# Optimization experiments

Measured on AMD Instinct MI355X. Metric: run time of the kernel, lower is better.

Reference implementation:

```python
import jax, jax.numpy as jnp
import numpy as np

B = 16       # number of point clouds
N_PER = 2048 # points per cloud
K = 16       # knn neighbors (loop=True -> self included as nearest)
NUM_CLASSES = 10


def _linear_params(key, fan_in, fan_out):
    # torch.nn.Linear default init: U(-1/sqrt(fan_in), 1/sqrt(fan_in))
    kw, kb = jax.random.split(key)
    s = 1.0 / np.sqrt(fan_in)
    W = jax.random.uniform(kw, (fan_in, fan_out), jnp.float32, -s, s)
    b = jax.random.uniform(kb, (fan_out,), jnp.float32, -s, s)
    return W, b


def setup_inputs() -> dict:
    key = jax.random.key(0)
    ks = jax.random.split(key, 7)
    pos = jax.random.normal(ks[0], (B * N_PER, 3), jnp.float32)
    batch = jnp.repeat(jnp.arange(B, dtype=jnp.int64), N_PER)  # sorted graph ids
    W1a, b1a = _linear_params(ks[1], 3 + 3, 32)   # conv1 mlp layer 1 (h=pos -> 3+3)
    W1b, b1b = _linear_params(ks[2], 32, 32)      # conv1 mlp layer 2
    W2a, b2a = _linear_params(ks[3], 32 + 3, 32)  # conv2 mlp layer 1
    W2b, b2b = _linear_params(ks[4], 32, 32)      # conv2 mlp layer 2
    Wc, bc = _linear_params(ks[5], 32, NUM_CLASSES)
    return dict(pos=pos, batch=batch,
                W1a=W1a, b1a=b1a, W1b=W1b, b1b=b1b,
                W2a=W2a, b2a=b2a, W2b=W2b, b2b=b2b,
                Wc=Wc, bc=bc)


def _knn_idx(p):
    # p: [n,3] -> [n,K] indices of K nearest points (self included, dist 0)
    d2 = jnp.sum((p[:, None, :] - p[None, :, :]) ** 2, axis=-1)  # [n,n]
    _, idx = jax.lax.top_k(-d2, K)
    return idx


def _pointnet_layer(h, p, idx, Wa, ba, Wb, bb):
    # single graph: h [n,C], p [n,3], idx [n,K]
    h_j = h[idx]                           # gather neighbor features [n,K,C]
    spatial = p[idx] - p[:, None, :]       # pos_j - pos_i [n,K,3]
    x = jnp.concatenate([h_j, spatial], axis=-1)
    x = jax.nn.relu(x @ Wa + ba) @ Wb + bb # per-edge MLP
    return jnp.max(x, axis=1)              # max aggregation over neighbors


def reference(pos, batch, W1a, b1a, W1b, b1b, W2a, b2a, W2b, b2b, Wc, bc):
    # batch is sorted with equal-sized graphs -> reshape to [B, n, 3]
    p = pos.reshape(B, N_PER, 3)
    idx = jax.vmap(_knn_idx)(p)  # [B, n, K] dynamic knn graph
    layer = jax.vmap(_pointnet_layer, in_axes=(0, 0, 0, None, None, None, None))
    h = jax.nn.relu(layer(p, p, idx, W1a, b1a, W1b, b1b))   # [B, n, 32]
    h = jax.nn.relu(layer(h, p, idx, W2a, b2a, W2b, b2b))   # [B, n, 32]
    g = jnp.max(h, axis=1)                                   # global_max_pool [B, 32]
    return g @ Wc + bc                                       # [B, num_classes]
```

## Files before the change

kernel.cpp:

```cpp
#include <hip/hip_runtime.h>
#include <hip/hip_bf16.h>
#include <cstdint>

#define NCLOUDS 16
#define N_PER   2048
#define KNN_K   16
#define CAP     48

typedef unsigned long long u64;
typedef __attribute__((ext_vector_type(8))) short bf16x8;
typedef __attribute__((ext_vector_type(4))) float f32x4;
#define INFF __builtin_inff()

template <int J>
__device__ __forceinline__ int ixor(int x) {
    if constexpr (J == 1)
        return __builtin_amdgcn_update_dpp(0, x, 0xB1, 0xF, 0xF, true);
    else if constexpr (J == 2)
        return __builtin_amdgcn_update_dpp(0, x, 0x4E, 0xF, 0xF, true);
    else if constexpr (J <= 16)
        return __builtin_amdgcn_ds_swizzle(x, (J << 10) | 0x1F);
    else
        return __shfl_xor(x, 32);
}
template <int J> __device__ __forceinline__ float fxor(float x) {
    return __int_as_float(ixor<J>(__float_as_int(x)));
}
template <int J> __device__ __forceinline__ u64 uxor(u64 x) {
    const int lo = ixor<J>((int)(x & 0xffffffffULL));
    const int hi = ixor<J>((int)(x >> 32));
    return ((u64)(unsigned)hi << 32) | (unsigned)lo;
}

__device__ __forceinline__ unsigned short f2bf(float f) {
    const unsigned u = __float_as_uint(f);
    const unsigned r = 0x7fffu + ((u >> 16) & 1u);
    return (unsigned short)((u + r) >> 16);
}

__global__ __launch_bounds__(512) void knn_kernel(const float* __restrict__ pos,
                                                  int* __restrict__ knn_out,
                                                  const float* __restrict__ W1a,
                                                  const float* __restrict__ b1a,
                                                  float* __restrict__ w1,
                                                  float* __restrict__ v1,
                                                  float* __restrict__ gbuf,
                                                  int* __restrict__ counter)
{
    __shared__ float qshare[3][32];
    __shared__ float smA[4][2][8][16];
    __shared__ u64   buf[4][8][CAP];
    __shared__ int   cnt[4][8];

    const int cloud = blockIdx.x >> 6;
    const int qblk  = blockIdx.x & 63;
    const int tid   = threadIdx.x;
    const int wave  = tid >> 6;
    const int lane  = tid & 63;
    const int H     = wave & 1;
    const int pr    = wave >> 1;

    const int b0 = cloud * N_PER;

    if (blockIdx.x == 0) {
        if (tid < NCLOUDS * 32) gbuf[tid] = 0.0f;
        if (tid == 0) *counter = 0;
    }

    if (tid < 32) {
        const float* qp = pos + (size_t)(b0 + qblk * 32 + tid) * 3;
        qshare[0][tid] = qp[0];
        qshare[1][tid] = qp[1];
        qshare[2][tid] = qp[2];
        ((int*)cnt)[tid] = 0;
    }

    float cx[16], cy[16], cz[16], sc[16];
#pragma unroll
    for (int jj = 0; jj < 16; ++jj) {
        const int c = H * 1024 + jj * 64 + lane;
        const float* p = pos + (size_t)(b0 + c) * 3;
        cx[jj] = p[0]; cy[jj] = p[1]; cz[jj] = p[2];
        sc[jj] = fmaf(cz[jj], cz[jj], fmaf(cy[jj], cy[jj], cx[jj] * cx[jj]));
    }
    __syncthreads();

#pragma unroll 1
    for (int t = 0; t < 4; ++t) {
        const int qg0 = pr * 8 + 2 * t, qg1 = qg0 + 1;
        const float Q0x = qshare[0][qg0], Q0y = qshare[1][qg0], Q0z = qshare[2][qg0];
        const float Q1x = qshare[0][qg1], Q1y = qshare[1][qg1], Q1z = qshare[2][qg1];
        const float A0x = -2.0f * Q0x, A0y = -2.0f * Q0y, A0z = -2.0f * Q0z;
        const float A1x = -2.0f * Q1x, A1y = -2.0f * Q1y, A1z = -2.0f * Q1z;
        float v0 = INFF, v1r = INFF;
#pragma unroll
        for (int jj = 0; jj < 16; ++jj) {
            float e0 = fmaf(cx[jj], A0x, sc[jj]);
            float e1 = fmaf(cx[jj], A1x, sc[jj]);
            e0 = fmaf(cy[jj], A0y, e0);  e1 = fmaf(cy[jj], A1y, e1);
            e0 = fmaf(cz[jj], A0z, e0);  e1 = fmaf(cz[jj], A1z, e1);
            v0 = fminf(v0, e0);          v1r = fminf(v1r, e1);
        }
#define FS(K, J) { const float o0 = fxor<J>(v0), o1 = fxor<J>(v1r);             \
                   const bool km = (((lane & J) == 0) == ((lane & K) == 0));    \
                   v0 = km ? fminf(v0, o0) : fmaxf(v0, o0);                     \
                   v1r = km ? fminf(v1r, o1) : fmaxf(v1r, o1); }
        FS(2,1)
        FS(4,2) FS(4,1)
        FS(8,4) FS(8,2) FS(8,1)
        FS(16,8) FS(16,4) FS(16,2) FS(16,1)
        FS(32,16) FS(32,8) FS(32,4) FS(32,2) FS(32,1)
        FS(64,32) FS(64,16) FS(64,8) FS(64,4) FS(64,2) FS(64,1)
#undef FS
        if (lane < 16) {
            smA[pr][H][2 * t][lane]     = v0;
            smA[pr][H][2 * t + 1][lane] = v1r;
        }
    }
    __syncthreads();

#pragma unroll 1
    for (int t = 0; t < 4; ++t) {
        const int q0 = 2 * t, q1 = q0 + 1;
        float a0 = -INFF, a1 = -INFF, b0v = -INFF, b1v = -INFF;
        if (lane > 0 && lane <= 16) {
            a0 = smA[pr][0][q0][lane - 1];
            a1 = smA[pr][0][q1][lane - 1];
        }
        if (lane < 16) {
            b0v = smA[pr][1][q0][15 - lane];
            b1v = smA[pr][1][q1][15 - lane];
        }
        float m0 = (lane <= 16) ? fmaxf(a0, b0v) : INFF;
        float m1 = (lane <= 16) ? fmaxf(a1, b1v) : INFF;
        m0 = fminf(m0, fxor<1>(m0));   m1 = fminf(m1, fxor<1>(m1));
        m0 = fminf(m0, fxor<2>(m0));   m1 = fminf(m1, fxor<2>(m1));
        m0 = fminf(m0, fxor<4>(m0));   m1 = fminf(m1, fxor<4>(m1));
        m0 = fminf(m0, fxor<8>(m0));   m1 = fminf(m1, fxor<8>(m1));
        m0 = fminf(m0, fxor<16>(m0));  m1 = fminf(m1, fxor<16>(m1));
        m0 = fminf(m0, fxor<32>(m0));  m1 = fminf(m1, fxor<32>(m1));

        const int qg0 = pr * 8 + q0, qg1 = pr * 8 + q1;
        const float Q0x = qshare[0][qg0], Q0y = qshare[1][qg0], Q0z = qshare[2][qg0];
        const float Q1x = qshare[0][qg1], Q1y = qshare[1][qg1], Q1z = qshare[2][qg1];
        const float qq0 = fmaf(Q0z, Q0z, fmaf(Q0y, Q0y, Q0x * Q0x));
        const float qq1 = fmaf(Q1z, Q1z, fmaf(Q1y, Q1y, Q1x * Q1x));
        const float T0 = (m0 + qq0) * (1.0f + 1e-5f) + 1e-4f;
        const float T1 = (m1 + qq1) * (1.0f + 1e-5f) + 1e-4f;

#pragma unroll
        for (int jj = 0; jj < 16; ++jj) {
            const int c = H * 1024 + jj * 64 + lane;
            const float dx0 = __fsub_rn(Q0x, cx[jj]);
            const float dy0 = __fsub_rn(Q0y, cy[jj]);
            const float dz0 = __fsub_rn(Q0z, cz[jj]);
            const float d20 = __fadd_rn(__fadd_rn(__fmul_rn(dx0, dx0), __fmul_rn(dy0, dy0)),
                                        __fmul_rn(dz0, dz0));
            if (d20 <= T0) {
                const int slot = atomicAdd(&cnt[pr][q0], 1);
                if (slot < CAP)
                    buf[pr][q0][slot] = ((u64)__float_as_uint(d20) << 32) | (unsigned)c;
            }
            const float dx1 = __fsub_rn(Q1x, cx[jj]);
            const float dy1 = __fsub_rn(Q1y, cy[jj]);
            const float dz1 = __fsub_rn(Q1z, cz[jj]);
            const float d21 = __fadd_rn(__fadd_rn(__fmul_rn(dx1, dx1), __fmul_rn(dy1, dy1)),
                                        __fmul_rn(dz1, dz1));
            if (d21 <= T1) {
                const int slot = atomicAdd(&cnt[pr][q1], 1);
                if (slot < CAP)
                    buf[pr][q1][slot] = ((u64)__float_as_uint(d21) << 32) | (unsigned)c;
            }
        }
    }
    __syncthreads();

#pragma unroll 1
    for (int s = 0; s < 2; ++s) {
        const int q0 = H * 4 + 2 * s, q1 = q0 + 1;
        const int n0 = min(cnt[pr][q0], CAP);
        const int n1 = min(cnt[pr][q1], CAP);
        u64 k0 = (lane < n0) ? buf[pr][q0][lane] : ~0ULL;
        u64 k1 = (lane < n1) ? buf[pr][q1][lane] : ~0ULL;
#define US(K, J) { const u64 o0 = uxor<J>(k0), o1 = uxor<J>(k1);                \
                   const bool km = (((lane & J) == 0) == ((lane & K) == 0));    \
                   const u64 l0 = k0 < o0 ? k0 : o0, h0 = k0 < o0 ? o0 : k0;    \
                   k0 = km ? l0 : h0;                                           \
                   const u64 l1 = k1 < o1 ? k1 : o1, h1 = k1 < o1 ? o1 : k1;    \
                   k1 = km ? l1 : h1; }
        US(2,1)
        US(4,2) US(4,1)
        US(8,4) US(8,2) US(8,1)
        US(16,8) US(16,4) US(16,2) US(16,1)
        US(32,16) US(32,8) US(32,4) US(32,2) US(32,1)
        US(64,32) US(64,16) US(64,8) US(64,4) US(64,2) US(64,1)
#undef US
        if (lane < KNN_K) {
            knn_out[((size_t)b0 + qblk * 32 + pr * 8 + q0) * KNN_K + lane] =
                b0 + (int)(unsigned)(k0 & 0xffffffffu);
            knn_out[((size_t)b0 + qblk * 32 + pr * 8 + q1) * KNN_K + lane] =
                b0 + (int)(unsigned)(k1 & 0xffffffffu);
        }
    }

    {
        const int pt = tid >> 4;
        const int kk = tid & 15;
        const int gp = b0 + qblk * 32 + pt;
        const float p0 = pos[3 * (size_t)gp + 0];
        const float p1 = pos[3 * (size_t)gp + 1];
        const float p2 = pos[3 * (size_t)gp + 2];
        float vA = 0.f, vB = 0.f;
        float wA = b1a[kk], wB = b1a[16 + kk];
#pragma unroll
        for (int d = 0; d < 3; ++d) {
            const float pd = d == 0 ? p0 : (d == 1 ? p1 : p2);
            wA = fmaf(pd, W1a[d * 32 + kk],        wA);
            wB = fmaf(pd, W1a[d * 32 + 16 + kk],   wB);
            vA = fmaf(pd, W1a[(3 + d) * 32 + kk],      vA);
            vB = fmaf(pd, W1a[(3 + d) * 32 + 16 + kk], vB);
        }
        w1[(size_t)gp * 32 + kk]      = wA + vA;
        w1[(size_t)gp * 32 + 16 + kk] = wB + vB;
        v1[(size_t)gp * 32 + kk]      = vA;
        v1[(size_t)gp * 32 + 16 + kk] = vB;
    }
}

template <int MODE>
__global__ __launch_bounds__(256) void layer_kernel(
    const int*   __restrict__ knn,
    const float* __restrict__ Wb, const float* __restrict__ bb,
    const float* __restrict__ w,  const float* __restrict__ v,
    const float* __restrict__ pos,
    const float* __restrict__ Wna, const float* __restrict__ bna,
    float* __restrict__ outA, float* __restrict__ outB,
    const float* __restrict__ Wc, const float* __restrict__ bc,
    float* __restrict__ gbuf, int* __restrict__ counter,
    float* __restrict__ out)
{
    __shared__ uint4 hidp[4][64][5];
    __shared__ float hs[16][32];
    __shared__ float gl[NCLOUDS * 32];
    __shared__ int   lastFlag;

    const int tid  = threadIdx.x;
    const int wv   = tid >> 6;
    const int lane = tid & 63;
    const int xcd   = blockIdx.x & 7;
    const int tt    = blockIdx.x >> 3;
    const int cloud = xcd * 2 + (tt & 1);
    const int ib    = tt >> 1;
    const int P0    = cloud * N_PER + ib * 16;
    const int k     = tid & 15;
    const int pl    = tid >> 4;
    const int p     = P0 + pl;
    const int j     = knn[(size_t)p * KNN_K + k];

    const float4* w4 = (const float4*)w;
    const float4* v4 = (const float4*)v;

    float hid[32];
#pragma unroll
    for (int i = 0; i < 8; ++i) {
        const float4 a = w4[(size_t)j * 8 + i];
        const float4 b = v4[(size_t)p * 8 + i];
        hid[4 * i + 0] = fmaxf(a.x - b.x, 0.0f);
        hid[4 * i + 1] = fmaxf(a.y - b.y, 0.0f);
        hid[4 * i + 2] = fmaxf(a.z - b.z, 0.0f);
        hid[4 * i + 3] = fmaxf(a.w - b.w, 0.0f);
    }

    const int kg = (lane >> 4) * 8;
    const int cl = lane & 15;
    bf16x8 bfr[2];
#pragma unroll
    for (int n = 0; n < 2; ++n)
#pragma unroll
        for (int jj = 0; jj < 8; ++jj)
            bfr[n][jj] = (short)f2bf(Wb[(kg + jj) * 32 + n * 16 + cl]);

    {
        uint4 pk[4];
#pragma unroll
        for (int q4 = 0; q4 < 4; ++q4) {
            unsigned a0 = (unsigned)f2bf(hid[8 * q4 + 0]) | ((unsigned)f2bf(hid[8 * q4 + 1]) << 16);
            unsigned a1 = (unsigned)f2bf(hid[8 * q4 + 2]) | ((unsigned)f2bf(hid[8 * q4 + 3]) << 16);
            unsigned a2 = (unsigned)f2bf(hid[8 * q4 + 4]) | ((unsigned)f2bf(hid[8 * q4 + 5]) << 16);
            unsigned a3 = (unsigned)f2bf(hid[8 * q4 + 6]) | ((unsigned)f2bf(hid[8 * q4 + 7]) << 16);
            pk[q4] = make_uint4(a0, a1, a2, a3);
        }
#pragma unroll
        for (int q4 = 0; q4 < 4; ++q4) hidp[wv][lane][q4] = pk[q4];
    }

    const f32x4 zero = {0.f, 0.f, 0.f, 0.f};
#pragma unroll
    for (int m = 0; m < 4; ++m) {
        const uint4 av = hidp[wv][m * 16 + cl][lane >> 4];
        const bf16x8 afr = __builtin_bit_cast(bf16x8, av);
        const f32x4 d0 = __builtin_amdgcn_mfma_f32_16x16x32_bf16(afr, bfr[0], zero, 0, 0, 0);
        const f32x4 d1 = __builtin_amdgcn_mfma_f32_16x16x32_bf16(afr, bfr[1], zero, 0, 0, 0);
        float m0 = fmaxf(fmaxf(d0[0], d0[1]), fmaxf(d0[2], d0[3]));
        float m1 = fmaxf(fmaxf(d1[0], d1[1]), fmaxf(d1[2], d1[3]));
        m0 = fmaxf(m0, fxor<16>(m0));  m1 = fmaxf(m1, fxor<16>(m1));
        m0 = fmaxf(m0, fxor<32>(m0));  m1 = fmaxf(m1, fxor<32>(m1));
        const int bp = wv * 4 + m;
        hs[bp][cl]      = fmaxf(bb[cl]      + m0, 0.0f);
        hs[bp][16 + cl] = fmaxf(bb[16 + cl] + m1, 0.0f);
    }
    __syncthreads();

    if constexpr (MODE == 1) {
        float accA = bna[k], accB = bna[16 + k];
#pragma unroll
        for (int c = 0; c < 32; ++c) {
            const float hc = hs[pl][c];
            accA = fmaf(hc, Wna[c * 32 + k],      accA);
            accB = fmaf(hc, Wna[c * 32 + 16 + k], accB);
        }
        float vA = 0.f, vB = 0.f;
#pragma unroll
        for (int d = 0; d < 3; ++d) {
            const float pd = pos[3 * (size_t)p + d];
            vA = fmaf(pd, Wna[(32 + d) * 32 + k],      vA);
            vB = fmaf(pd, Wna[(32 + d) * 32 + 16 + k], vB);
        }
        outA[(size_t)p * 32 + k]      = accA + vA;
        outA[(size_t)p * 32 + 16 + k] = accB + vB;
        outB[(size_t)p * 32 + k]      = vA;
        outB[(size_t)p * 32 + 16 + k] = vB;
    } else {
        if (tid < 32) {
            float m = hs[0][tid];
#pragma unroll
            for (int p2 = 1; p2 < 16; ++p2) m = fmaxf(m, hs[p2][tid]);
            atomicMax((int*)&gbuf[cloud * 32 + tid], __float_as_int(m));
        }
        __syncthreads();
        if (tid == 0) {
            __threadfence();
            lastFlag = (atomicAdd(counter, 1) == (int)gridDim.x - 1);
        }
        __syncthreads();
        if (lastFlag) {
            for (int t = tid; t < NCLOUDS * 32; t += 256)
                gl[t] = __int_as_float(atomicMax((int*)&gbuf[t], 0));
            __syncthreads();
            if (tid < NCLOUDS * 10) {
                const int cl2 = tid / 10, cls = tid - cl2 * 10;
                float s2 = bc[cls];
#pragma unroll
                for (int c = 0; c < 32; ++c)
                    s2 = fmaf(gl[cl2 * 32 + c], Wc[c * 10 + cls], s2);
                out[tid] = s2;
            }
        }
    }
}

extern "C" void kernel_launch(void* const* d_in, const int* in_sizes, int n_in,
                              void* d_out, int out_size, void* d_ws, size_t ws_size,
                              hipStream_t stream)
{
    const float* pos = (const float*)d_in[0];
    const float* W1a = (const float*)d_in[2];
    const float* b1a = (const float*)d_in[3];
    const float* W1b = (const float*)d_in[4];
    const float* b1b = (const float*)d_in[5];
    const float* W2a = (const float*)d_in[6];
    const float* b2a = (const float*)d_in[7];
    const float* W2b = (const float*)d_in[8];
    const float* b2b = (const float*)d_in[9];
    const float* Wc  = (const float*)d_in[10];
    const float* bc  = (const float*)d_in[11];

    int*   knn     = (int*)d_ws;
    float* w1      = (float*)((char*)d_ws + (size_t)(2  << 20));
    float* v1      = (float*)((char*)d_ws + (size_t)(6  << 20));
    float* w2      = (float*)((char*)d_ws + (size_t)(10 << 20));
    float* v2      = (float*)((char*)d_ws + (size_t)(14 << 20));
    float* gbuf    = (float*)((char*)d_ws + (size_t)(18 << 20));
    int*   counter = (int*)((char*)d_ws + (size_t)(18 << 20) + 4096);
    float* out     = (float*)d_out;

    const int npts = NCLOUDS * N_PER;

    knn_kernel<<<dim3(NCLOUDS * 64), dim3(512), 0, stream>>>(
        pos, knn, W1a, b1a, w1, v1, gbuf, counter);
    layer_kernel<1><<<dim3(npts * KNN_K / 256), dim3(256), 0, stream>>>(
        knn, W1b, b1b, w1, v1, pos, W2a, b2a, w2, v2,
        nullptr, nullptr, nullptr, nullptr, nullptr);
    layer_kernel<2><<<dim3(npts * KNN_K / 256), dim3(256), 0, stream>>>(
        knn, W2b, b2b, w2, v2, pos, nullptr, nullptr, nullptr, nullptr,
        Wc, bc, gbuf, counter, out);
}
```

Measured before the change: 122.8 us.

## Prefilter kNN candidates with expanded-form distance and sort float keys only

Adds a cheap expanded-form distance prefilter, using |c|^2 - 2q·c via FMAs, before the exact rounded distance and atomic insert. This cuts the arithmetic per candidate. The 64-bit key bitonic sort is replaced by a 32-bit float-only sort to find the 16th distance. Indices are then emitted by ballot/popcount compaction, with a tie-break loop that picks equal-distance entries by smallest index. This removes half the cross-lane traffic in the sort, but adds a serial tie-handling loop and relies on the prefilter margin being conservative.

Result: slower. 151.4 us (+23.4%).

```diff
diff --git a/kernel.cpp b/kernel.cpp
--- a/kernel.cpp
+++ b/kernel.cpp
@@ -25,11 +25,6 @@
 }
 template <int J> __device__ __forceinline__ float fxor(float x) {
     return __int_as_float(ixor<J>(__float_as_int(x)));
-}
-template <int J> __device__ __forceinline__ u64 uxor(u64 x) {
-    const int lo = ixor<J>((int)(x & 0xffffffffULL));
-    const int hi = ixor<J>((int)(x >> 32));
-    return ((u64)(unsigned)hi << 32) | (unsigned)lo;
 }
 
 __device__ __forceinline__ unsigned short f2bf(float f) {
@@ -143,33 +138,47 @@
         const int qg0 = pr * 8 + q0, qg1 = pr * 8 + q1;
         const float Q0x = qshare[0][qg0], Q0y = qshare[1][qg0], Q0z = qshare[2][qg0];
         const float Q1x = qshare[0][qg1], Q1y = qshare[1][qg1], Q1z = qshare[2][qg1];
+        const float A0x = -2.0f * Q0x, A0y = -2.0f * Q0y, A0z = -2.0f * Q0z;
+        const float A1x = -2.0f * Q1x, A1y = -2.0f * Q1y, A1z = -2.0f * Q1z;
         const float qq0 = fmaf(Q0z, Q0z, fmaf(Q0y, Q0y, Q0x * Q0x));
         const float qq1 = fmaf(Q1z, Q1z, fmaf(Q1y, Q1y, Q1x * Q1x));
         const float T0 = (m0 + qq0) * (1.0f + 1e-5f) + 1e-4f;
         const float T1 = (m1 + qq1) * (1.0f + 1e-5f) + 1e-4f;
+        const float F0 = T0 + 1e-4f;
+        const float F1 = T1 + 1e-4f;
 
 #pragma unroll
         for (int jj = 0; jj < 16; ++jj) {
             const int c = H * 1024 + jj * 64 + lane;
-            const float dx0 = __fsub_rn(Q0x, cx[jj]);
-            const float dy0 = __fsub_rn(Q0y, cy[jj]);
-            const float dz0 = __fsub_rn(Q0z, cz[jj]);
-            const float d20 = __fadd_rn(__fadd_rn(__fmul_rn(dx0, dx0), __fmul_rn(dy0, dy0)),
-                                        __fmul_rn(dz0, dz0));
-            if (d20 <= T0) {
-                const int slot = atomicAdd(&cnt[pr][q0], 1);
-                if (slot < CAP)
-                    buf[pr][q0][slot] = ((u64)__float_as_uint(d20) << 32) | (unsigned)c;
+            float e0 = fmaf(cx[jj], A0x, sc[jj]);
+            e0 = fmaf(cy[jj], A0y, e0);
+            e0 = fmaf(cz[jj], A0z, e0);
+            if (e0 + qq0 <= F0) {
+                const float dx0 = __fsub_rn(Q0x, cx[jj]);
+                const float dy0 = __fsub_rn(Q0y, cy[jj]);
+                const float dz0 = __fsub_rn(Q0z, cz[jj]);
+                const float d20 = __fadd_rn(__fadd_rn(__fmul_rn(dx0, dx0), __fmul_rn(dy0, dy0)),
+                                            __fmul_rn(dz0, dz0));
+                if (d20 <= T0) {
+                    const int slot = atomicAdd(&cnt[pr][q0], 1);
+                    if (slot < CAP)
+                        buf[pr][q0][slot] = ((u64)__float_as_uint(d20) << 32) | (unsigned)c;
+                }
             }
-            const float dx1 = __fsub_rn(Q1x, cx[jj]);
-            const float dy1 = __fsub_rn(Q1y, cy[jj]);
-            const float dz1 = __fsub_rn(Q1z, cz[jj]);
-            const float d21 = __fadd_rn(__fadd_rn(__fmul_rn(dx1, dx1), __fmul_rn(dy1, dy1)),
-                                        __fmul_rn(dz1, dz1));
-            if (d21 <= T1) {
-                const int slot = atomicAdd(&cnt[pr][q1], 1);
-                if (slot < CAP)
-                    buf[pr][q1][slot] = ((u64)__float_as_uint(d21) << 32) | (unsigned)c;
+            float e1 = fmaf(cx[jj], A1x, sc[jj]);
+            e1 = fmaf(cy[jj], A1y, e1);
+            e1 = fmaf(cz[jj], A1z, e1);
+            if (e1 + qq1 <= F1) {
+                const float dx1 = __fsub_rn(Q1x, cx[jj]);
+                const float dy1 = __fsub_rn(Q1y, cy[jj]);
+                const float dz1 = __fsub_rn(Q1z, cz[jj]);
+                const float d21 = __fadd_rn(__fadd_rn(__fmul_rn(dx1, dx1), __fmul_rn(dy1, dy1)),
+                                            __fmul_rn(dz1, dz1));
+                if (d21 <= T1) {
+                    const int slot = atomicAdd(&cnt[pr][q1], 1);
+                    if (slot < CAP)
+                        buf[pr][q1][slot] = ((u64)__float_as_uint(d21) << 32) | (unsigned)c;
+                }
             }
         }
     }
@@ -180,26 +189,70 @@
         const int q0 = H * 4 + 2 * s, q1 = q0 + 1;
         const int n0 = min(cnt[pr][q0], CAP);
         const int n1 = min(cnt[pr][q1], CAP);
-        u64 k0 = (lane < n0) ? buf[pr][q0][lane] : ~0ULL;
-        u64 k1 = (lane < n1) ? buf[pr][q1][lane] : ~0ULL;
-#define US(K, J) { const u64 o0 = uxor<J>(k0), o1 = uxor<J>(k1);                \
+        float d0 = INFF, d1 = INFF;
+        int   i0 = 0x7fffffff, i1 = 0x7fffffff;
+        if (lane < n0) {
+            const u64 kk = buf[pr][q0][lane];
+            d0 = __uint_as_float((unsigned)(kk >> 32));
+            i0 = (int)(unsigned)(kk & 0xffffffffu);
+        }
+        if (lane < n1) {
+            const u64 kk = buf[pr][q1][lane];
+            d1 = __uint_as_float((unsigned)(kk >> 32));
+            i1 = (int)(unsigned)(kk & 0xffffffffu);
+        }
+        float a0 = d0, a1 = d1;
+#define FS(K, J) { const float o0 = fxor<J>(a0), o1 = fxor<J>(a1);              \
                    const bool km = (((lane & J) == 0) == ((lane & K) == 0));    \
-                   const u64 l0 = k0 < o0 ? k0 : o0, h0 = k0 < o0 ? o0 : k0;    \
-                   k0 = km ? l0 : h0;                                           \
-                   const u64 l1 = k1 < o1 ? k1 : o1, h1 = k1 < o1 ? o1 : k1;    \
-                   k1 = km ? l1 : h1; }
-        US(2,1)
-        US(4,2) US(4,1)
-        US(8,4) US(8,2) US(8,1)
-        US(16,8) US(16,4) US(16,2) US(16,1)
-        US(32,16) US(32,8) US(32,4) US(32,2) US(32,1)
-        US(64,32) US(64,16) US(64,8) US(64,4) US(64,2) US(64,1)
-#undef US
-        if (lane < KNN_K) {
-            knn_out[((size_t)b0 + qblk * 32 + pr * 8 + q0) * KNN_K + lane] =
-                b0 + (int)(unsigned)(k0 & 0xffffffffu);
-            knn_out[((size_t)b0 + qblk * 32 + pr * 8 + q1) * KNN_K + lane] =
-                b0 + (int)(unsigned)(k1 & 0xffffffffu);
+                   a0 = km ? fminf(a0, o0) : fmaxf(a0, o0);                     \
+                   a1 = km ? fminf(a1, o1) : fmaxf(a1, o1); }
+        FS(2,1)
+        FS(4,2) FS(4,1)
+        FS(8,4) FS(8,2) FS(8,1)
+        FS(16,8) FS(16,4) FS(16,2) FS(16,1)
+        FS(32,16) FS(32,8) FS(32,4) FS(32,2) FS(32,1)
+        FS(64,32) FS(64,16) FS(64,8) FS(64,4) FS(64,2) FS(64,1)
+#undef FS
+        const float d16_0 = __shfl(a0, KNN_K - 1);
+        const float d16_1 = __shfl(a1, KNN_K - 1);
+
+        int* outp0 = knn_out + ((size_t)b0 + qblk * 32 + pr * 8 + q0) * KNN_K;
+        int* outp1 = knn_out + ((size_t)b0 + qblk * 32 + pr * 8 + q1) * KNN_K;
+        const u64 lmask = (1ull << lane) - 1;
+
+        const u64 blt0 = __ballot(d0 < d16_0);
+        const u64 blt1 = __ballot(d1 < d16_1);
+        if (d0 < d16_0) outp0[__popcll(blt0 & lmask)] = b0 + i0;
+        if (d1 < d16_1) outp1[__popcll(blt1 & lmask)] = b0 + i1;
+        const int c10 = (int)__popcll(blt0);
+        const int c11 = (int)__popcll(blt1);
+        u64 beq0 = __ballot(d0 == d16_0);
+        u64 beq1 = __ballot(d1 == d16_1);
+#pragma unroll 1
+        for (int it = c10; it < KNN_K; ++it) {
+            int cand = ((beq0 >> lane) & 1) ? i0 : 0x7fffffff;
+            cand = min(cand, ixor<1>(cand));
+            cand = min(cand, ixor<2>(cand));
+            cand = min(cand, ixor<4>(cand));
+            cand = min(cand, ixor<8>(cand));
+            cand = min(cand, ixor<16>(cand));
+            cand = min(cand, ixor<32>(cand));
+            const bool own = ((beq0 >> lane) & 1) && (i0 == cand);
+            if (own) outp0[it] = b0 + i0;
+            beq0 &= ~__ballot(own);
+        }
+#pragma unroll 1
+        for (int it = c11; it < KNN_K; ++it) {
+            int cand = ((beq1 >> lane) & 1) ? i1 : 0x7fffffff;
+            cand = min(cand, ixor<1>(cand));
+            cand = min(cand, ixor<2>(cand));
+            cand = min(cand, ixor<4>(cand));
+            cand = min(cand, ixor<8>(cand));
+            cand = min(cand, ixor<16>(cand));
+            cand = min(cand, ixor<32>(cand));
+            const bool own = ((beq1 >> lane) & 1) && (i1 == cand);
+            if (own) outp1[it] = b0 + i1;
+            beq1 &= ~__ballot(own);
         }
     }
 
```
